# Kernel tuning notes

Hardware: AMD Instinct MI355X
Metric: run time of the kernel (lower is better)

The kernel has to match this reference:

```python
import jax, jax.numpy as jnp
import numpy as np

LMBDA = 0.1
ALPHA = 0.05
NBIT = 4


def setup_inputs() -> dict:
    key = jax.random.key(0)
    k1, k2 = jax.random.split(key)
    shape = (4096, 16384)
    weight = jax.random.normal(k1, shape, dtype=jnp.float32) * 0.05
    Qn, Qp = -2 ** (NBIT - 1), 2 ** (NBIT - 1) - 1
    q_int = jax.random.randint(k2, shape, Qn, Qp + 1)  # bins in [-8, 7]
    weight_q = (q_int.astype(jnp.float32)) * ALPHA
    alpha = jnp.full((1,), ALPHA, dtype=jnp.float32)
    return {"weight": weight, "weight_q": weight_q, "nbit": NBIT, "alpha": alpha}


def reference(weight, weight_q, nbit, alpha):
    # dampening_loss with aggregation='mean', scaled by lmbda (single quant layer)
    Qn = -2 ** (nbit - 1)
    Qp = 2 ** (nbit - 1) - 1
    nbins = Qp - Qn + 1
    a = alpha.reshape(())

    # (w_q.detach() - w)^2 mean  (detach is a no-op in fwd)
    loss = jnp.mean((weight_q - weight) ** 2)

    # Fused histogram pass: per-bin count / sum / sumsq of `weight`,
    # keyed by the quant bin of weight_q (exact-equality mask in original).
    bin_id = jnp.round(weight_q / a).astype(jnp.int32) - Qn  # [0, nbins)
    w = weight.reshape(-1)
    b = bin_id.reshape(-1)
    cnt = jax.ops.segment_sum(jnp.ones_like(w), b, num_segments=nbins)
    s = jax.ops.segment_sum(w, b, num_segments=nbins)
    ss = jax.ops.segment_sum(w * w, b, num_segments=nbins)

    # unbiased variance per bin, only added when count > 1 (as in torch.var)
    denom_n = jnp.maximum(cnt, 1.0)
    denom_nm1 = jnp.maximum(cnt - 1.0, 1.0)
    var = (ss - s * s / denom_n) / denom_nm1
    loss = loss + jnp.sum(jnp.where(cnt > 1.0, var, 0.0))

    return LMBDA * loss
```

## Files before the change

kernel.cpp:

```cpp
#include <hip/hip_runtime.h>

#define NBINS 16
#define TPB   256
#define GRID  1280


__global__ __launch_bounds__(TPB, 5) void binreg_main(
    const float* __restrict__ w, const float* __restrict__ wq,
    const float* __restrict__ alpha_p, const int* __restrict__ nbit_p,
    float* __restrict__ partial, long long n)
{
    __shared__ float2 sv[NBINS * TPB];

    const int tid = threadIdx.x;

    #pragma unroll
    for (int k = 0; k < NBINS; ++k) sv[k * TPB + tid] = make_float2(0.0f, 0.0f);

    const float inv_a = 1.0f / alpha_p[0];
    const int   qoff  = 1 << (nbit_p[0] - 1);

    const long long n4     = n >> 2;
    const long long stride = (long long)GRID * TPB;
    const float4* w4 = (const float4*)w;
    const float4* q4 = (const float4*)wq;

    float sq = 0.0f;
    unsigned long long nib = 0ull;
    int cnt[NBINS];
    #pragma unroll
    for (int k = 0; k < NBINS; ++k) cnt[k] = 0;
    int fc = 3;

    long long i = (long long)blockIdx.x * TPB + tid;
    bool valid = i < n4;
    float4 a, b;
    if (valid) { a = w4[i]; b = q4[i]; }

    while (valid) {
        long long ni = i + stride;
        bool nvalid = ni < n4;
        float4 an, bn;
        if (nvalid) { an = w4[ni]; bn = q4[ni]; }

        float d0 = b.x - a.x, d1 = b.y - a.y, d2 = b.z - a.z, d3 = b.w - a.w;
        sq += d0 * d0 + d1 * d1 + d2 * d2 + d3 * d3;

        int b0 = ((int)rintf(b.x * inv_a) + qoff) & (NBINS - 1);
        int b1 = ((int)rintf(b.y * inv_a) + qoff) & (NBINS - 1);
        int b2 = ((int)rintf(b.z * inv_a) + qoff) & (NBINS - 1);
        int b3 = ((int)rintf(b.w * inv_a) + qoff) & (NBINS - 1);

        nib += (1ull << (b0 << 2)) + (1ull << (b1 << 2))
             + (1ull << (b2 << 2)) + (1ull << (b3 << 2));
        if (--fc == 0) {
            #pragma unroll
            for (int k = 0; k < NBINS; ++k)
                cnt[k] += (int)((nib >> (k * 4)) & 0xFull);
            nib = 0ull; fc = 3;
        }

        int i0 = (b0 << 8) + tid;
        int i1 = (b1 << 8) + tid;
        int i2 = (b2 << 8) + tid;
        int i3 = (b3 << 8) + tid;

        { float2 t = sv[i0]; t.x += a.x; t.y += a.x * a.x; sv[i0] = t; }
        { float2 t = sv[i1]; t.x += a.y; t.y += a.y * a.y; sv[i1] = t; }
        { float2 t = sv[i2]; t.x += a.z; t.y += a.z * a.z; sv[i2] = t; }
        { float2 t = sv[i3]; t.x += a.w; t.y += a.w * a.w; sv[i3] = t; }

        i = ni; valid = nvalid; a = an; b = bn;
    }

    for (long long t4 = (n4 << 2) + (long long)blockIdx.x * TPB + tid; t4 < n; t4 += stride) {
        float av = w[t4], bv = wq[t4];
        float d = bv - av;
        sq += d * d;
        int bb = ((int)rintf(bv * inv_a) + qoff) & (NBINS - 1);
        nib += 1ull << (bb << 2);
        #pragma unroll
        for (int k = 0; k < NBINS; ++k)
            cnt[k] += (int)((nib >> (k * 4)) & 0xFull);
        nib = 0ull;
        int ii = (bb << 8) + tid;
        float2 t = sv[ii]; t.x += av; t.y += av * av; sv[ii] = t;
    }
    #pragma unroll
    for (int k = 0; k < NBINS; ++k)
        cnt[k] += (int)((nib >> (k * 4)) & 0xFull);

    for (int off = 32; off; off >>= 1) sq += __shfl_down(sq, off, 64);
    #pragma unroll
    for (int k = 0; k < NBINS; ++k)
        for (int off = 32; off; off >>= 1) cnt[k] += __shfl_down(cnt[k], off, 64);

    const int wave = tid >> 6, lane = tid & 63;
    __syncthreads();

    for (int c = wave; c < 32; c += 4) {
        const int bin = c & 15;
        float v = 0.0f;
        #pragma unroll
        for (int r = 0; r < TPB / 64; ++r) {
            float2 t = sv[(bin << 8) + r * 64 + lane];
            v += (c < 16) ? t.x : t.y;
        }
        for (int off = 32; off; off >>= 1) v += __shfl_down(v, off, 64);
        if (lane == 0) partial[c * GRID + blockIdx.x] = v;
    }
    __syncthreads();

    float* stage = (float*)sv;
    if (lane == 0) {
        #pragma unroll
        for (int k = 0; k < NBINS; ++k) stage[wave * NBINS + k] = (float)cnt[k];
        stage[64 + wave] = sq;
    }
    __syncthreads();

    if (tid < NBINS) {
        float v = stage[tid] + stage[16 + tid] + stage[32 + tid] + stage[48 + tid];
        partial[(32 + tid) * GRID + blockIdx.x] = v;
    }
    if (tid == 16)
        partial[48 * GRID + blockIdx.x] =
            (stage[64] + stage[65]) + (stage[66] + stage[67]);
}

__global__ __launch_bounds__(TPB) void binreg_final1(
    const float* __restrict__ partial, float* __restrict__ cells)
{
    const int c = blockIdx.x;
    const int tid = threadIdx.x, wave = tid >> 6, lane = tid & 63;
    __shared__ float wsum[4];

    float v = 0.0f;
    for (int r = tid; r < GRID; r += TPB) v += partial[c * GRID + r];
    for (int off = 32; off; off >>= 1) v += __shfl_down(v, off, 64);
    if (lane == 0) wsum[wave] = v;
    __syncthreads();
    if (tid == 0) cells[c] = (wsum[0] + wsum[1]) + (wsum[2] + wsum[3]);
}

__global__ void binreg_final2(const float* __restrict__ cells,
                              float* __restrict__ out, long long n)
{
    if (threadIdx.x == 0 && blockIdx.x == 0) {
        float loss = cells[48] / (float)n;
        #pragma unroll
        for (int b = 0; b < NBINS; ++b) {
            float s   = cells[b];
            float ss  = cells[16 + b];
            float cnt = cells[32 + b];
            if (cnt > 1.0f)
                loss += (ss - s * s / cnt) / (cnt - 1.0f);
        }
        out[0] = 0.1f * loss;
    }
}

extern "C" void kernel_launch(void* const* d_in, const int* in_sizes, int n_in,
                              void* d_out, int out_size, void* d_ws, size_t ws_size,
                              hipStream_t stream)
{
    const float* w     = (const float*)d_in[0];
    const float* wq    = (const float*)d_in[1];
    const int*   nbit  = (const int*)d_in[2];
    const float* alpha = (const float*)d_in[3];
    float* out     = (float*)d_out;
    float* partial = (float*)d_ws;
    float* cells   = partial + 49 * GRID;
    long long n = (long long)in_sizes[0];

    binreg_main  <<<GRID, TPB, 0, stream>>>(w, wq, alpha, nbit, partial, n);
    binreg_final1<<<49,   TPB, 0, stream>>>(partial, cells);
    binreg_final2<<<1,    64,  0, stream>>>(cells, out, n);
}
```

Measured before the change: 542.8 us.

## Replace LDS per-bin histogram with register accumulators via predicated selects

Drops the shared-memory float2 per-thread-per-bin histogram and its read-modify-write traffic. Each thread instead keeps 16 sum and 16 sum-of-squares registers, updated by select-and-FMA across all bins. This removes LDS latency and bank conflicts but adds about 16x more VALU work per element and extra register pressure. The grid shrinks to 1024 blocks, the manual next-iteration prefetch is dropped, and the per-block reduction is simplified into one staged shuffle pass.

Result: slower. 561.2 us (+3.4%).

```diff
diff --git a/kernel.cpp b/kernel.cpp
--- a/kernel.cpp
+++ b/kernel.cpp
@@ -2,46 +2,37 @@
 
 #define NBINS 16
 #define TPB   256
-#define GRID  1280
+#define GRID  1024
 
 
-__global__ __launch_bounds__(TPB, 5) void binreg_main(
+__global__ __launch_bounds__(TPB) void binreg_main(
     const float* __restrict__ w, const float* __restrict__ wq,
     const float* __restrict__ alpha_p, const int* __restrict__ nbit_p,
     float* __restrict__ partial, long long n)
 {
-    __shared__ float2 sv[NBINS * TPB];
-
     const int tid = threadIdx.x;
-
-    #pragma unroll
-    for (int k = 0; k < NBINS; ++k) sv[k * TPB + tid] = make_float2(0.0f, 0.0f);
 
     const float inv_a = 1.0f / alpha_p[0];
     const int   qoff  = 1 << (nbit_p[0] - 1);
+
+    float accS [NBINS];
+    float accSS[NBINS];
+    int   cnt  [NBINS];
+    #pragma unroll
+    for (int k = 0; k < NBINS; ++k) { accS[k] = 0.f; accSS[k] = 0.f; cnt[k] = 0; }
+
+    float sq = 0.0f;
+    unsigned long long nib = 0ull;
+    int fc = 3;
 
     const long long n4     = n >> 2;
     const long long stride = (long long)GRID * TPB;
     const float4* w4 = (const float4*)w;
     const float4* q4 = (const float4*)wq;
 
-    float sq = 0.0f;
-    unsigned long long nib = 0ull;
-    int cnt[NBINS];
-    #pragma unroll
-    for (int k = 0; k < NBINS; ++k) cnt[k] = 0;
-    int fc = 3;
-
-    long long i = (long long)blockIdx.x * TPB + tid;
-    bool valid = i < n4;
-    float4 a, b;
-    if (valid) { a = w4[i]; b = q4[i]; }
-
-    while (valid) {
-        long long ni = i + stride;
-        bool nvalid = ni < n4;
-        float4 an, bn;
-        if (nvalid) { an = w4[ni]; bn = q4[ni]; }
+    for (long long i = (long long)blockIdx.x * TPB + tid; i < n4; i += stride) {
+        float4 a = w4[i];
+        float4 b = q4[i];
 
         float d0 = b.x - a.x, d1 = b.y - a.y, d2 = b.z - a.z, d3 = b.w - a.w;
         sq += d0 * d0 + d1 * d1 + d2 * d2 + d3 * d3;
@@ -60,17 +51,18 @@
             nib = 0ull; fc = 3;
         }
 
-        int i0 = (b0 << 8) + tid;
-        int i1 = (b1 << 8) + tid;
-        int i2 = (b2 << 8) + tid;
-        int i3 = (b3 << 8) + tid;
-
-        { float2 t = sv[i0]; t.x += a.x; t.y += a.x * a.x; sv[i0] = t; }
-        { float2 t = sv[i1]; t.x += a.y; t.y += a.y * a.y; sv[i1] = t; }
-        { float2 t = sv[i2]; t.x += a.z; t.y += a.z * a.z; sv[i2] = t; }
-        { float2 t = sv[i3]; t.x += a.w; t.y += a.w * a.w; sv[i3] = t; }
-
-        i = ni; valid = nvalid; a = an; b = bn;
+        #pragma unroll
+        for (int k = 0; k < NBINS; ++k) {
+            float s0 = (b0 == k) ? a.x : 0.0f;
+            float s1 = (b1 == k) ? a.y : 0.0f;
+            float s2 = (b2 == k) ? a.z : 0.0f;
+            float s3 = (b3 == k) ? a.w : 0.0f;
+            accS [k] += (s0 + s1) + (s2 + s3);
+            accSS[k] = fmaf(s0, s0, accSS[k]);
+            accSS[k] = fmaf(s1, s1, accSS[k]);
+            accSS[k] = fmaf(s2, s2, accSS[k]);
+            accSS[k] = fmaf(s3, s3, accSS[k]);
+        }
     }
 
     for (long long t4 = (n4 << 2) + (long long)blockIdx.x * TPB + tid; t4 < n; t4 += stride) {
@@ -80,52 +72,33 @@
         int bb = ((int)rintf(bv * inv_a) + qoff) & (NBINS - 1);
         nib += 1ull << (bb << 2);
         #pragma unroll
-        for (int k = 0; k < NBINS; ++k)
-            cnt[k] += (int)((nib >> (k * 4)) & 0xFull);
-        nib = 0ull;
-        int ii = (bb << 8) + tid;
-        float2 t = sv[ii]; t.x += av; t.y += av * av; sv[ii] = t;
+        for (int k = 0; k < NBINS; ++k) {
+            float s0 = (bb == k) ? av : 0.0f;
+            accS [k] += s0;
+            accSS[k] = fmaf(s0, s0, accSS[k]);
+        }
     }
     #pragma unroll
     for (int k = 0; k < NBINS; ++k)
         cnt[k] += (int)((nib >> (k * 4)) & 0xFull);
 
-    for (int off = 32; off; off >>= 1) sq += __shfl_down(sq, off, 64);
+    __shared__ float stage[4 * 49];
+    const int wave = tid >> 6, lane = tid & 63;
+
     #pragma unroll
-    for (int k = 0; k < NBINS; ++k)
-        for (int off = 32; off; off >>= 1) cnt[k] += __shfl_down(cnt[k], off, 64);
-
-    const int wave = tid >> 6, lane = tid & 63;
-    __syncthreads();
-
-    for (int c = wave; c < 32; c += 4) {
-        const int bin = c & 15;
-        float v = 0.0f;
-        #pragma unroll
-        for (int r = 0; r < TPB / 64; ++r) {
-            float2 t = sv[(bin << 8) + r * 64 + lane];
-            v += (c < 16) ? t.x : t.y;
-        }
+    for (int c = 0; c < 49; ++c) {
+        float v = (c < 16) ? accS[c]
+                : (c < 32) ? accSS[c - 16]
+                : (c < 48) ? (float)cnt[c - 32]
+                : sq;
         for (int off = 32; off; off >>= 1) v += __shfl_down(v, off, 64);
-        if (lane == 0) partial[c * GRID + blockIdx.x] = v;
+        if (lane == 0) stage[wave * 49 + c] = v;
     }
     __syncthreads();
 
-    float* stage = (float*)sv;
-    if (lane == 0) {
-        #pragma unroll
-        for (int k = 0; k < NBINS; ++k) stage[wave * NBINS + k] = (float)cnt[k];
-        stage[64 + wave] = sq;
-    }
-    __syncthreads();
-
-    if (tid < NBINS) {
-        float v = stage[tid] + stage[16 + tid] + stage[32 + tid] + stage[48 + tid];
-        partial[(32 + tid) * GRID + blockIdx.x] = v;
-    }
-    if (tid == 16)
-        partial[48 * GRID + blockIdx.x] =
-            (stage[64] + stage[65]) + (stage[66] + stage[67]);
+    if (tid < 49)
+        partial[tid * GRID + blockIdx.x] =
+            (stage[tid] + stage[49 + tid]) + (stage[98 + tid] + stage[147 + tid]);
 }
 
 __global__ __launch_bounds__(TPB) void binreg_final1(
```
